# Optimization experiments

Hardware: AMD Instinct MI355X
Metric: run time of the kernel (lower is better)

## Reference

```python
import jax, jax.numpy as jnp
import numpy as np

V, D, L, H, FF, MAXLEN, M = 128, 512, 4, 8, 2048, 1024, 4
B, T = 2, 1024
DK = D // H
EPS = 1e-5  # F.layer_norm default


def setup_inputs() -> dict:
    key = jax.random.key(0)
    ks = jax.random.split(key, 10)
    x = jax.random.randint(ks[0], (B, T), 0, V)
    inp = {
        'x': x,
        'tok_emb': 0.02 * jax.random.normal(ks[1], (M, V, D), jnp.float32),
        'pos_emb': 0.02 * jax.random.normal(ks[2], (M, MAXLEN, D), jnp.float32),
        'ln1_w': jnp.ones((L, M, D), jnp.float32),
        'ln1_b': jnp.zeros((L, M, D), jnp.float32),
        'qkv_w': jax.random.normal(ks[3], (L, M, 3 * D, D), jnp.float32) * (1.0 / np.sqrt(D)),
        'qkv_b': jnp.zeros((L, M, 3 * D), jnp.float32),
        'out_w': jax.random.normal(ks[4], (L, M, D, D), jnp.float32) * (1.0 / np.sqrt(D)),
        'out_b': jnp.zeros((L, M, D), jnp.float32),
        'ln2_w': jnp.ones((L, M, D), jnp.float32),
        'ln2_b': jnp.zeros((L, M, D), jnp.float32),
        'ff1_w': jax.random.normal(ks[5], (L, M, FF, D), jnp.float32) * (1.0 / np.sqrt(D)),
        'ff1_b': jnp.zeros((L, M, FF), jnp.float32),
        'ff2_w': jax.random.normal(ks[6], (L, M, D, FF), jnp.float32) * (1.0 / np.sqrt(FF)),
        'ff2_b': jnp.zeros((L, M, D), jnp.float32),
        'lnf_w': jnp.ones((M, D), jnp.float32),
        'lnf_b': jnp.zeros((M, D), jnp.float32),
        'head_w': jax.random.normal(ks[7], (M, V, D), jnp.float32) * (1.0 / np.sqrt(D)),
        'head_b': jnp.zeros((M, V), jnp.float32),
    }
    return inp


def _layernorm(h, w, b):
    # h: [M,B,T,D], w/b: [M,D]
    mu = h.mean(-1, keepdims=True)
    var = ((h - mu) ** 2).mean(-1, keepdims=True)
    return (h - mu) / jnp.sqrt(var + EPS) * w[:, None, None, :] + b[:, None, None, :]


def reference(x, tok_emb, pos_emb, ln1_w, ln1_b, qkv_w, qkv_b, out_w, out_b,
              ln2_w, ln2_b, ff1_w, ff1_b, ff2_w, ff2_b, lnf_w, lnf_b, head_w, head_b):
    Bx, Tx = x.shape
    # token + positional embedding, batched over the model axis -> [M,B,T,D]
    h = tok_emb[:, x] + pos_emb[:, None, :Tx, :]
    mask = jnp.tril(jnp.ones((Tx, Tx), bool))  # causal
    scale = 1.0 / np.sqrt(DK).astype(np.float32)
    for l in range(L):
        n = _layernorm(h, ln1_w[l], ln1_b[l])
        qkv = jnp.einsum('mbtd,mfd->mbtf', n, qkv_w[l]) + qkv_b[l][:, None, None, :]
        # (M,B,T,H,3*DK) -> (M,B,H,T,3*DK); chunk last dim into q,k,v (matches torch chunk)
        qkv = qkv.reshape(h.shape[0], Bx, Tx, H, 3 * DK).transpose(0, 1, 3, 2, 4)
        q, k, v = jnp.split(qkv, 3, axis=-1)
        s = jnp.einsum('mbhtd,mbhsd->mbhts', q, k) * scale
        s = jnp.where(mask, s, -jnp.inf)
        a = jax.nn.softmax(s, axis=-1)
        o = jnp.einsum('mbhts,mbhsd->mbhtd', a, v)
        o = o.transpose(0, 1, 3, 2, 4).reshape(h.shape[0], Bx, Tx, D)
        o = jnp.einsum('mbtd,med->mbte', o, out_w[l]) + out_b[l][:, None, None, :]
        h = h + o
        n = _layernorm(h, ln2_w[l], ln2_b[l])
        f = jax.nn.relu(jnp.einsum('mbtd,mfd->mbtf', n, ff1_w[l]) + ff1_b[l][:, None, None, :])
        f = jnp.einsum('mbtf,mdf->mbtd', f, ff2_w[l]) + ff2_b[l][:, None, None, :]
        h = h + f
    h = _layernorm(h, lnf_w, lnf_b)
    logits = jnp.einsum('mbtd,mvd->mbtv', h, head_w) + head_b[:, None, None, :]
    return logits.transpose(1, 0, 2, 3)  # (B, model_count, T, V) like torch.stack(dim=1)
```

## Files before the change

### kernel.cpp

```cpp
#include <hip/hip_runtime.h>

#define M_  4
#define B_  2
#define T_  1024
#define D_  512
#define V_  128
#define L_  4
#define H_  8
#define FF_ 2048
#define DK_ 64
#define BT_ (B_*T_)
#define EPS_ 1e-5f
#define QSCALE_ 0.18033688f

typedef __attribute__((ext_vector_type(8))) short  bf16x8;
typedef __attribute__((ext_vector_type(4))) float  f32x4;
typedef __attribute__((ext_vector_type(8))) ushort ushort8v;

__device__ __forceinline__ float b2f(ushort u) {
  union { unsigned int i; float f; } c; c.i = ((unsigned int)u) << 16; return c.f;
}
__device__ __forceinline__ ushort f2b(float f) {
  union { float f; unsigned int i; } c; c.f = f;
  return (ushort)((c.i + 0x7FFFu + ((c.i >> 16) & 1u)) >> 16);
}
__device__ __forceinline__ void gload_lds16(const void* g, void* l) {
  __builtin_amdgcn_global_load_lds((const __attribute__((address_space(1))) unsigned int*)g,
                                   (__attribute__((address_space(3))) unsigned int*)l, 16, 0, 0);
}

__global__ __launch_bounds__(128)
void k_embed(const int* __restrict__ x, const float* __restrict__ tok,
             const float* __restrict__ pos, ushort* __restrict__ h)
{
  const int t = blockIdx.x, b = blockIdx.y, m = blockIdx.z;
  const int d = threadIdx.x * 4;
  const int xv = x[b*T_ + t];
  const float4 tv = *(const float4*)&tok[((size_t)m*V_ + xv)*D_ + d];
  const float4 pv = *(const float4*)&pos[((size_t)m*1024 + t)*D_ + d];
  ushort4 r;
  r.x = f2b(tv.x + pv.x); r.y = f2b(tv.y + pv.y);
  r.z = f2b(tv.z + pv.z); r.w = f2b(tv.w + pv.w);
  *(ushort4*)&h[(((size_t)m*B_ + b)*T_ + t)*D_ + d] = r;
}

#define NQ4_ 786432
#define NO4_ 262144
#define NF4_ 1048576
#define LBLK_ 12288
#define LSLAB_ 12582912
__global__ __launch_bounds__(256)
void k_cvt_all(const float* __restrict__ qkv_w, const float* __restrict__ out_w,
               const float* __restrict__ ff1_w, const float* __restrict__ ff2_w,
               const float* __restrict__ head_w, ushort* __restrict__ wall)
{
  const int bx = blockIdx.x;
  const float* s; ushort* d;
  long i;
  if (bx < 4*LBLK_) {
    const int l  = bx / LBLK_;
    i = (long)(bx % LBLK_)*256 + threadIdx.x;
    ushort* base = wall + (size_t)l*LSLAB_;
    if (i < NQ4_)                  { s = qkv_w + (size_t)l*3145728; d = base; }
    else if (i < NQ4_+NO4_)        { s = out_w + (size_t)l*1048576; d = base + 3145728; i -= NQ4_; }
    else if (i < NQ4_+NO4_+NF4_)   { s = ff1_w + (size_t)l*4194304; d = base + 4194304; i -= NQ4_+NO4_; }
    else                           { s = ff2_w + (size_t)l*4194304; d = base + 8388608; i -= NQ4_+NO4_+NF4_; }
  } else {
    i = (long)(bx - 4*LBLK_)*256 + threadIdx.x;
    s = head_w; d = wall + (size_t)4*LSLAB_;
  }
  const float4 a = ((const float4*)s)[i];
  ushort4 o;
  o.x = f2b(a.x); o.y = f2b(a.y); o.z = f2b(a.z); o.w = f2b(a.w);
  ((ushort4*)d)[i] = o;
}

__global__ __launch_bounds__(256)
void k_ln(const ushort* __restrict__ x, const float* __restrict__ w,
          const float* __restrict__ bb, ushort* __restrict__ y)
{
  const int row  = blockIdx.x * 4 + (threadIdx.x >> 6);
  const int lane = threadIdx.x & 63;
  const int m = row >> 11;
  const ushort8v xv = *(const ushort8v*)&x[(size_t)row*D_ + lane*8];
  float v[8];
  #pragma unroll
  for (int k = 0; k < 8; ++k) v[k] = b2f(xv[k]);
  float s = 0.f, s2 = 0.f;
  #pragma unroll
  for (int k = 0; k < 8; ++k) { s += v[k]; s2 += v[k]*v[k]; }
  #pragma unroll
  for (int off = 1; off < 64; off <<= 1) {
    s  += __shfl_xor(s, off);
    s2 += __shfl_xor(s2, off);
  }
  const float mu   = s * (1.0f/D_);
  const float var  = s2 * (1.0f/D_) - mu*mu;
  const float rstd = rsqrtf(var + EPS_);
  const float* wp = w + m*D_ + lane*8;
  const float* bp = bb + m*D_ + lane*8;
  const float4 w0 = *(const float4*)wp, w1 = *(const float4*)(wp+4);
  const float4 b0 = *(const float4*)bp, b1 = *(const float4*)(bp+4);
  const float wr[8] = {w0.x,w0.y,w0.z,w0.w,w1.x,w1.y,w1.z,w1.w};
  const float br[8] = {b0.x,b0.y,b0.z,b0.w,b1.x,b1.y,b1.z,b1.w};
  ushort8v o;
  #pragma unroll
  for (int k = 0; k < 8; ++k) o[k] = f2b((v[k]-mu)*rstd*wr[k] + br[k]);
  *(ushort8v*)&y[(size_t)row*D_ + lane*8] = o;
}

template<int OUTBF, int ACT, int RES, int HEADOUT, int SPLITV>
__global__ __launch_bounds__(256)
void k_gemm(const ushort* __restrict__ A, const ushort* __restrict__ W,
            const float* __restrict__ bias, const ushort* __restrict__ resid,
            void* __restrict__ C, ushort* __restrict__ vt, int RR, int NN, int KK)
{
  const int m  = blockIdx.z;
  const int r0 = blockIdx.x * 128;
  const int c0 = blockIdx.y * 128;
  const ushort* Am = A + (size_t)m*RR*KK;
  const ushort* Wm = W + (size_t)m*NN*KK;

  __shared__ ushort As[2][128*64];
  __shared__ ushort Bs[2][128*64];

  const int tid  = threadIdx.x;
  const int lane = tid & 63;
  const int wave = tid >> 6;
  const int wr = wave >> 1, wc = wave & 1;
  const int fr = lane & 15;
  const int fq = lane >> 4;

  f32x4 acc[4][4];
  #pragma unroll
  for (int i = 0; i < 4; ++i)
    #pragma unroll
    for (int j = 0; j < 4; ++j)
      acc[i][j] = (f32x4){0.f,0.f,0.f,0.f};

  #pragma unroll
  for (int i = 0; i < 4; ++i) {
    const int c = i*256 + tid;
    const int row = c >> 3, ch = c & 7;
    const int sch = ch ^ (row & 7);
    gload_lds16(Am + (size_t)(r0+row)*KK + sch*8, (ushort*)As[0] + (size_t)c*8);
    gload_lds16(Wm + (size_t)(c0+row)*KK + sch*8, (ushort*)Bs[0] + (size_t)c*8);
  }
  __syncthreads();

  const int NK = KK >> 6;
  for (int kt = 0; kt < NK; ++kt) {
    const int cur = kt & 1;

    if (kt + 1 < NK) {
      const int k0 = (kt + 1) * 64;
      #pragma unroll
      for (int i = 0; i < 4; ++i) {
        const int c = i*256 + tid;
        const int row = c >> 3, ch = c & 7;
        const int sch = ch ^ (row & 7);
        gload_lds16(Am + (size_t)(r0+row)*KK + k0 + sch*8, (ushort*)As[cur^1] + (size_t)c*8);
        gload_lds16(Wm + (size_t)(c0+row)*KK + k0 + sch*8, (ushort*)Bs[cur^1] + (size_t)c*8);
      }
      asm volatile("s_waitcnt vmcnt(8)" ::: "memory");
    } else {
      asm volatile("s_waitcnt vmcnt(0)" ::: "memory");
    }
    __builtin_amdgcn_sched_barrier(0);
    __builtin_amdgcn_s_barrier();

    #pragma unroll
    for (int kk = 0; kk < 2; ++kk) {
      bf16x8 af[4], bfv[4];
      #pragma unroll
      for (int i = 0; i < 4; ++i) {
        const int rowA = wr*64 + i*16 + fr;
        af[i]  = *(const bf16x8*)&As[cur][rowA*64 + (((kk*4 + fq) ^ (rowA & 7))*8)];
        const int rowB = wc*64 + i*16 + fr;
        bfv[i] = *(const bf16x8*)&Bs[cur][rowB*64 + (((kk*4 + fq) ^ (rowB & 7))*8)];
      }
      #pragma unroll
      for (int i = 0; i < 4; ++i)
        #pragma unroll
        for (int j = 0; j < 4; ++j)
          acc[i][j] = __builtin_amdgcn_mfma_f32_16x16x32_bf16(af[i], bfv[j], acc[i][j], 0, 0, 0);
    }
    __builtin_amdgcn_s_barrier();
  }

  const int colb = c0 + wc*64 + fr;
  float bi[4];
  #pragma unroll
  for (int j = 0; j < 4; ++j) bi[j] = bias[(size_t)m*NN + colb + j*16];

  if (SPLITV) {
    #pragma unroll
    for (int i = 0; i < 4; ++i) {
      const int row0 = r0 + wr*64 + i*16 + fq*4;
      const int mbg = (blockIdx.z)*B_ + (row0 >> 10);
      const int t0  = row0 & 1023;
      #pragma unroll
      for (int j = 0; j < 4; ++j) {
        const int col = colb + j*16;
        const int hh2 = col / 192;
        const int sub = col - hh2*192;
        float v0 = acc[i][j][0] + bi[j];
        float v1 = acc[i][j][1] + bi[j];
        float v2 = acc[i][j][2] + bi[j];
        float v3 = acc[i][j][3] + bi[j];
        if (sub >= 128) {
          ushort4 pk;
          pk.x = f2b(v0); pk.y = f2b(v1); pk.z = f2b(v2); pk.w = f2b(v3);
          *(ushort4*)&vt[(((size_t)mbg*8 + hh2)*64 + (sub-128))*1024 + t0] = pk;
        } else {
          if (sub < 64) { v0 *= QSCALE_; v1 *= QSCALE_; v2 *= QSCALE_; v3 *= QSCALE_; }
          ushort* cp = (ushort*)C + ((size_t)m*RR + row0)*NN + col;
          cp[0*NN] = f2b(v0); cp[1*NN] = f2b(v1); cp[2*NN] = f2b(v2); cp[3*NN] = f2b(v3);
        }
      }
    }
  } else {
    #pragma unroll
    for (int i = 0; i < 4; ++i) {
      #pragma unroll
      for (int r = 0; r < 4; ++r) {
        const int row = r0 + wr*64 + i*16 + fq*4 + r;
        #pragma unroll
        for (int j = 0; j < 4; ++j) {
          float val = acc[i][j][r] + bi[j];
          if (ACT) val = fmaxf(val, 0.0f);
          const int col = colb + j*16;
          size_t oidx;
          if (HEADOUT) {
            const int b = row >> 10, t = row & 1023;
            oidx = (((size_t)b*M_ + m)*T_ + t)*V_ + col;
          } else {
            oidx = ((size_t)m*RR + row)*NN + col;
          }
          float v2 = val;
          if (RES) v2 += b2f(resid[oidx]);
          if (OUTBF) ((ushort*)C)[oidx] = f2b(v2);
          else       ((float*)C)[oidx]  = v2;
        }
      }
    }
  }
}

__global__ __launch_bounds__(256)
void k_attn_mfma(const ushort* __restrict__ qkvb, const ushort* __restrict__ vt,
                 ushort* __restrict__ o)
{
  const int hh   = blockIdx.x;
  const int pair = blockIdx.y;
  const int mbg  = blockIdx.z;

  __shared__ ushort Qs[64*64];
  __shared__ ushort Ks[2][64*64];
  __shared__ ushort Vs[2][64*64];
  __shared__ ushort Ps[4][16*80];

  const int tid  = threadIdx.x;
  const int lane = tid & 63;
  const int wave = tid >> 6;
  const int fr = lane & 15;
  const int fq = lane >> 4;

  const ushort* qk_base = qkvb + (size_t)mbg*T_*(3*D_) + hh*(3*DK_);
  const ushort* vt_base = vt + ((size_t)(mbg*8 + hh)*64)*1024;

  #pragma unroll 1
  for (int pass = 0; pass < 2; ++pass) {
    const int qb = pass ? (15 - pair) : pair;

    #pragma unroll
    for (int i = 0; i < 2; ++i) {
      const int c = wave*128 + i*64 + lane;
      const int row = c >> 3, ch = c & 7;
      const int sch = (ch ^ (row & 7)) * 8;
      gload_lds16(qk_base + (size_t)(qb*64 + row)*(3*D_) + sch,
                  (ushort*)Qs + (size_t)(wave*128 + i*64)*8);
      gload_lds16(qk_base + (size_t)row*(3*D_) + DK_ + sch,
                  (ushort*)Ks[0] + (size_t)(wave*128 + i*64)*8);
      gload_lds16(vt_base + (size_t)row*1024 + sch,
                  (ushort*)Vs[0] + (size_t)(wave*128 + i*64)*8);
    }
    __syncthreads();

    bf16x8 aQ[2];
    #pragma unroll
    for (int kc = 0; kc < 2; ++kc) {
      const int qrow = wave*16 + fr;
      aQ[kc] = *(const bf16x8*)&Qs[qrow*64 + (((kc*4 + fq) ^ (qrow&7))*8)];
    }

    float m_q = -3.0e38f, l_q = 0.0f;
    f32x4 Of[4];
    #pragma unroll
    for (int j = 0; j < 4; ++j) Of[j] = (f32x4){0.f,0.f,0.f,0.f};

    const int qrow_abs0 = qb*64 + wave*16 + fq*4;

    auto tile = [&](int kb, bool DIAG, bool PRE) {
      const int cur = kb & 1;
      if (PRE) {
        #pragma unroll
        for (int i = 0; i < 2; ++i) {
          const int c = wave*128 + i*64 + lane;
          const int row = c >> 3, ch = c & 7;
          const int sch = (ch ^ (row & 7)) * 8;
          gload_lds16(qk_base + (size_t)((kb+1)*64 + row)*(3*D_) + DK_ + sch,
                      (ushort*)Ks[cur^1] + (size_t)(wave*128 + i*64)*8);
          gload_lds16(vt_base + (size_t)row*1024 + (kb+1)*64 + sch,
                      (ushort*)Vs[cur^1] + (size_t)(wave*128 + i*64)*8);
        }
        asm volatile("s_waitcnt vmcnt(4)" ::: "memory");
      } else {
        asm volatile("s_waitcnt vmcnt(0)" ::: "memory");
      }
      __builtin_amdgcn_sched_barrier(0);
      __builtin_amdgcn_s_barrier();

      f32x4 acc[4];
      #pragma unroll
      for (int j = 0; j < 4; ++j) acc[j] = (f32x4){0.f,0.f,0.f,0.f};
      __builtin_amdgcn_s_setprio(1);
      #pragma unroll
      for (int kc = 0; kc < 2; ++kc) {
        #pragma unroll
        for (int j = 0; j < 4; ++j) {
          const int krow = j*16 + fr;
          const bf16x8 bK = *(const bf16x8*)&Ks[cur][krow*64 + (((kc*4 + fq) ^ (krow&7))*8)];
          acc[j] = __builtin_amdgcn_mfma_f32_16x16x32_bf16(bK, aQ[kc], acc[j], 0, 0, 0);
        }
      }
      __builtin_amdgcn_s_setprio(0);

      float sv[16];
      #pragma unroll
      for (int j = 0; j < 4; ++j)
        #pragma unroll
        for (int r = 0; r < 4; ++r) {
          float v = acc[j][r];
          if (DIAG && (j*16 + fq*4 + r) > (wave*16 + fr)) v = -3.0e38f;
          sv[j*4+r] = v;
        }
      float a0 = fmaxf(fmaxf(sv[0],  sv[1]),  sv[2]);
      float a1 = fmaxf(fmaxf(sv[3],  sv[4]),  sv[5]);
      float a2 = fmaxf(fmaxf(sv[6],  sv[7]),  sv[8]);
      float a3 = fmaxf(fmaxf(sv[9],  sv[10]), sv[11]);
      float a4 = fmaxf(fmaxf(sv[12], sv[13]), sv[14]);
      float rm = fmaxf(fmaxf(fmaxf(a0, a1), fmaxf(a2, a3)), fmaxf(a4, sv[15]));
      rm = fmaxf(rm, __shfl_xor(rm, 16));
      rm = fmaxf(rm, __shfl_xor(rm, 32));
      if (!__all(rm - m_q <= 8.0f)) {
        const float mn = fmaxf(m_q, rm);
        const float sc = exp2f(m_q - mn);
        m_q = mn;
        l_q *= sc;
        float scr[4];
        #pragma unroll
        for (int r = 0; r < 4; ++r) scr[r] = __shfl(sc, fq*4 + r);
        #pragma unroll
        for (int j = 0; j < 4; ++j)
          #pragma unroll
          for (int r = 0; r < 4; ++r) Of[j][r] *= scr[r];
      }
      float p[16];
      #pragma unroll
      for (int i2 = 0; i2 < 16; ++i2) p[i2] = exp2f(sv[i2] - m_q);
      float s0 = (p[0]+p[1]) + (p[2]+p[3]);
      float s1 = (p[4]+p[5]) + (p[6]+p[7]);
      float s2 = (p[8]+p[9]) + (p[10]+p[11]);
      float s3 = (p[12]+p[13]) + (p[14]+p[15]);
      float rs = (s0+s1) + (s2+s3);
      rs += __shfl_xor(rs, 16);
      rs += __shfl_xor(rs, 32);
      l_q += rs;

      #pragma unroll
      for (int j = 0; j < 4; ++j) {
        unsigned int lo, hi;
        asm("v_cvt_pk_bf16_f32 %0, %1, %2" : "=v"(lo) : "v"(p[j*4+0]), "v"(p[j*4+1]));
        asm("v_cvt_pk_bf16_f32 %0, %1, %2" : "=v"(hi) : "v"(p[j*4+2]), "v"(p[j*4+3]));
        const int idx = (fr*80 + j*16 + fq*4) ^ ((fr>>2)<<4);
        *(unsigned int*)&Ps[wave][idx]     = lo;
        *(unsigned int*)&Ps[wave][idx + 2] = hi;
      }

      __builtin_amdgcn_s_setprio(1);
      #pragma unroll
      for (int kc = 0; kc < 2; ++kc) {
        const int pidx = fr*80 + kc*32 + fq*8;
        const bf16x8 pa = *(const bf16x8*)&Ps[wave][pidx ^ ((fr>>2)<<4)];
        #pragma unroll
        for (int j = 0; j < 4; ++j) {
          const int vrow = j*16 + fr;
          const bf16x8 bV = *(const bf16x8*)&Vs[cur][vrow*64 + (((kc*4 + fq) ^ (vrow&7))*8)];
          Of[j] = __builtin_amdgcn_mfma_f32_16x16x32_bf16(pa, bV, Of[j], 0, 0, 0);
        }
      }
      __builtin_amdgcn_s_setprio(0);
      __builtin_amdgcn_s_barrier();
    };

    for (int kb = 0; kb < qb; ++kb) tile(kb, false, true);
    tile(qb, true, false);

    const float linv = 1.0f / l_q;
    float inv[4];
    #pragma unroll
    for (int r = 0; r < 4; ++r) inv[r] = __shfl(linv, fq*4 + r);
    #pragma unroll
    for (int r = 0; r < 4; ++r) {
      ushort* op = o + ((size_t)mbg*T_ + (qrow_abs0 + r))*D_ + hh*DK_ + fr;
      #pragma unroll
      for (int j = 0; j < 4; ++j)
        op[j*16] = f2b(Of[j][r] * inv[r]);
    }
  }
}

extern "C" void kernel_launch(void* const* d_in, const int* in_sizes, int n_in,
                              void* d_out, int out_size, void* d_ws, size_t ws_size,
                              hipStream_t stream)
{
  const int*   x       = (const int*)  d_in[0];
  const float* tok_emb = (const float*)d_in[1];
  const float* pos_emb = (const float*)d_in[2];
  const float* ln1_w   = (const float*)d_in[3];
  const float* ln1_b   = (const float*)d_in[4];
  const float* qkv_w   = (const float*)d_in[5];
  const float* qkv_b   = (const float*)d_in[6];
  const float* out_w   = (const float*)d_in[7];
  const float* out_b   = (const float*)d_in[8];
  const float* ln2_w   = (const float*)d_in[9];
  const float* ln2_b   = (const float*)d_in[10];
  const float* ff1_w   = (const float*)d_in[11];
  const float* ff1_b   = (const float*)d_in[12];
  const float* ff2_w   = (const float*)d_in[13];
  const float* ff2_b   = (const float*)d_in[14];
  const float* lnf_w   = (const float*)d_in[15];
  const float* lnf_b   = (const float*)d_in[16];
  const float* head_w  = (const float*)d_in[17];
  const float* head_b  = (const float*)d_in[18];
  float* outp = (float*)d_out;

  const size_t HS = (size_t)M_*B_*T_*D_;
  ushort* h     = (ushort*)d_ws;
  ushort* nb    = h + HS;
  ushort* qkvb  = nb + HS;
  ushort* ob    = qkvb + (size_t)M_*B_*T_*3*D_;
  ushort* fb    = qkvb;
  ushort* vtb   = ob + HS;
  ushort* wall  = vtb + HS;
  ushort* wh    = wall + (size_t)4*LSLAB_;

  const int ROWS = M_*B_*T_;

  k_cvt_all<<<4*LBLK_ + 256, 256, 0, stream>>>(qkv_w, out_w, ff1_w, ff2_w, head_w, wall);
  k_embed<<<dim3(T_, B_, M_), 128, 0, stream>>>(x, tok_emb, pos_emb, h);

  for (int l = 0; l < L_; ++l) {
    ushort* wq  = wall + (size_t)l*LSLAB_;
    ushort* wo  = wq  + 3145728;
    ushort* wf1 = wo  + 1048576;
    ushort* wf2 = wf1 + 4194304;

    k_ln<<<ROWS/4, 256, 0, stream>>>(h, ln1_w + l*M_*D_, ln1_b + l*M_*D_, nb);

    k_gemm<1,0,0,0,1><<<dim3(BT_/128, (3*D_)/128, M_), 256, 0, stream>>>(
        nb, wq, qkv_b + l*M_*3*D_, nullptr, qkvb, vtb, BT_, 3*D_, D_);

    k_attn_mfma<<<dim3(H_, T_/128, M_*B_), 256, 0, stream>>>(qkvb, vtb, ob);

    k_gemm<1,0,1,0,0><<<dim3(BT_/128, D_/128, M_), 256, 0, stream>>>(
        ob, wo, out_b + l*M_*D_, h, h, nullptr, BT_, D_, D_);

    k_ln<<<ROWS/4, 256, 0, stream>>>(h, ln2_w + l*M_*D_, ln2_b + l*M_*D_, nb);

    k_gemm<1,1,0,0,0><<<dim3(BT_/128, FF_/128, M_), 256, 0, stream>>>(
        nb, wf1, ff1_b + l*M_*FF_, nullptr, fb, nullptr, BT_, FF_, D_);

    k_gemm<1,0,1,0,0><<<dim3(BT_/128, D_/128, M_), 256, 0, stream>>>(
        fb, wf2, ff2_b + l*M_*D_, h, h, nullptr, BT_, D_, FF_);
  }

  k_ln<<<ROWS/4, 256, 0, stream>>>(h, lnf_w, lnf_b, nb);
  k_gemm<0,0,0,1,0><<<dim3(BT_/128, V_/128, M_), 256, 0, stream>>>(
      nb, wh, head_b, nullptr, outp, nullptr, BT_, V_, D_);
}
```

Measured before the change: 580.1 us.

## Fuse fp32-to-bf16 weight conversion into GEMM B-tile loading

Removes the separate up-front kernel that converted all weights to bf16. Each GEMM now loads fp32 weight tiles into registers, converts them, and writes them to LDS after the MFMA stage, while A tiles still go direct to LDS. This drops one full read and write pass over all weights. In exchange, each GEMM block reads twice the weight bytes, and the register staging adds pressure and waitcnt complexity; weights are re-read once per row block.

Measured after the change: 744.8 us. +28.4%, slower.

```diff
diff --git a/kernel.cpp b/kernel.cpp
--- a/kernel.cpp
+++ b/kernel.cpp
@@ -42,37 +42,6 @@
   r.x = f2b(tv.x + pv.x); r.y = f2b(tv.y + pv.y);
   r.z = f2b(tv.z + pv.z); r.w = f2b(tv.w + pv.w);
   *(ushort4*)&h[(((size_t)m*B_ + b)*T_ + t)*D_ + d] = r;
-}
-
-#define NQ4_ 786432
-#define NO4_ 262144
-#define NF4_ 1048576
-#define LBLK_ 12288
-#define LSLAB_ 12582912
-__global__ __launch_bounds__(256)
-void k_cvt_all(const float* __restrict__ qkv_w, const float* __restrict__ out_w,
-               const float* __restrict__ ff1_w, const float* __restrict__ ff2_w,
-               const float* __restrict__ head_w, ushort* __restrict__ wall)
-{
-  const int bx = blockIdx.x;
-  const float* s; ushort* d;
-  long i;
-  if (bx < 4*LBLK_) {
-    const int l  = bx / LBLK_;
-    i = (long)(bx % LBLK_)*256 + threadIdx.x;
-    ushort* base = wall + (size_t)l*LSLAB_;
-    if (i < NQ4_)                  { s = qkv_w + (size_t)l*3145728; d = base; }
-    else if (i < NQ4_+NO4_)        { s = out_w + (size_t)l*1048576; d = base + 3145728; i -= NQ4_; }
-    else if (i < NQ4_+NO4_+NF4_)   { s = ff1_w + (size_t)l*4194304; d = base + 4194304; i -= NQ4_+NO4_; }
-    else                           { s = ff2_w + (size_t)l*4194304; d = base + 8388608; i -= NQ4_+NO4_+NF4_; }
-  } else {
-    i = (long)(bx - 4*LBLK_)*256 + threadIdx.x;
-    s = head_w; d = wall + (size_t)4*LSLAB_;
-  }
-  const float4 a = ((const float4*)s)[i];
-  ushort4 o;
-  o.x = f2b(a.x); o.y = f2b(a.y); o.z = f2b(a.z); o.w = f2b(a.w);
-  ((ushort4*)d)[i] = o;
 }
 
 __global__ __launch_bounds__(256)
@@ -111,7 +80,7 @@
 
 template<int OUTBF, int ACT, int RES, int HEADOUT, int SPLITV>
 __global__ __launch_bounds__(256)
-void k_gemm(const ushort* __restrict__ A, const ushort* __restrict__ W,
+void k_gemm(const ushort* __restrict__ A, const float* __restrict__ W,
             const float* __restrict__ bias, const ushort* __restrict__ resid,
             void* __restrict__ C, ushort* __restrict__ vt, int RR, int NN, int KK)
 {
@@ -119,7 +88,7 @@
   const int r0 = blockIdx.x * 128;
   const int c0 = blockIdx.y * 128;
   const ushort* Am = A + (size_t)m*RR*KK;
-  const ushort* Wm = W + (size_t)m*NN*KK;
+  const float*  Wm = W + (size_t)m*NN*KK;
 
   __shared__ ushort As[2][128*64];
   __shared__ ushort Bs[2][128*64];
@@ -138,34 +107,62 @@
     for (int j = 0; j < 4; ++j)
       acc[i][j] = (f32x4){0.f,0.f,0.f,0.f};
 
-  #pragma unroll
-  for (int i = 0; i < 4; ++i) {
-    const int c = i*256 + tid;
-    const int row = c >> 3, ch = c & 7;
-    const int sch = ch ^ (row & 7);
-    gload_lds16(Am + (size_t)(r0+row)*KK + sch*8, (ushort*)As[0] + (size_t)c*8);
-    gload_lds16(Wm + (size_t)(c0+row)*KK + sch*8, (ushort*)Bs[0] + (size_t)c*8);
-  }
-  __syncthreads();
+  float4 br[8];
+
+  auto issueA = [&](int kt, int buf) {
+    const int k0 = kt * 64;
+    #pragma unroll
+    for (int i = 0; i < 4; ++i) {
+      const int c = i*256 + tid;
+      const int row = c >> 3, ch = c & 7;
+      const int sch = ch ^ (row & 7);
+      gload_lds16(Am + (size_t)(r0+row)*KK + k0 + sch*8, (ushort*)As[buf] + (size_t)c*8);
+    }
+  };
+  auto issueB = [&](int kt) {
+    const int k0 = kt * 64;
+    #pragma unroll
+    for (int i = 0; i < 4; ++i) {
+      const int c = i*256 + tid;
+      const int row = c >> 3, ch = c & 7;
+      const int sch = ch ^ (row & 7);
+      const float* p = Wm + (size_t)(c0+row)*KK + k0 + sch*8;
+      br[2*i]   = *(const float4*)p;
+      br[2*i+1] = *(const float4*)(p + 4);
+    }
+  };
+  auto writeB = [&](int buf) {
+    #pragma unroll
+    for (int i = 0; i < 4; ++i) {
+      const int c = i*256 + tid;
+      ushort8v t;
+      t[0]=f2b(br[2*i].x);   t[1]=f2b(br[2*i].y);
+      t[2]=f2b(br[2*i].z);   t[3]=f2b(br[2*i].w);
+      t[4]=f2b(br[2*i+1].x); t[5]=f2b(br[2*i+1].y);
+      t[6]=f2b(br[2*i+1].z); t[7]=f2b(br[2*i+1].w);
+      *(ushort8v*)&Bs[buf][(size_t)c*8] = t;
+    }
+  };
+
+  issueB(0);
+  __builtin_amdgcn_sched_barrier(0);
+  issueA(0, 0);
+  asm volatile("s_waitcnt vmcnt(4)" ::: "memory");
+  writeB(0);
 
   const int NK = KK >> 6;
   for (int kt = 0; kt < NK; ++kt) {
     const int cur = kt & 1;
 
     if (kt + 1 < NK) {
-      const int k0 = (kt + 1) * 64;
-      #pragma unroll
-      for (int i = 0; i < 4; ++i) {
-        const int c = i*256 + tid;
-        const int row = c >> 3, ch = c & 7;
-        const int sch = ch ^ (row & 7);
-        gload_lds16(Am + (size_t)(r0+row)*KK + k0 + sch*8, (ushort*)As[cur^1] + (size_t)c*8);
-        gload_lds16(Wm + (size_t)(c0+row)*KK + k0 + sch*8, (ushort*)Bs[cur^1] + (size_t)c*8);
-      }
-      asm volatile("s_waitcnt vmcnt(8)" ::: "memory");
+      issueB(kt + 1);
+      __builtin_amdgcn_sched_barrier(0);
+      issueA(kt + 1, cur ^ 1);
+      asm volatile("s_waitcnt vmcnt(12)" ::: "memory");
     } else {
       asm volatile("s_waitcnt vmcnt(0)" ::: "memory");
     }
+    asm volatile("s_waitcnt lgkmcnt(0)" ::: "memory");
     __builtin_amdgcn_sched_barrier(0);
     __builtin_amdgcn_s_barrier();
 
@@ -186,6 +183,11 @@
           acc[i][j] = __builtin_amdgcn_mfma_f32_16x16x32_bf16(af[i], bfv[j], acc[i][j], 0, 0, 0);
     }
     __builtin_amdgcn_s_barrier();
+
+    if (kt + 1 < NK) {
+      asm volatile("s_waitcnt vmcnt(4)" ::: "memory");
+      writeB(cur ^ 1);
+    }
   }
 
   const int colb = c0 + wc*64 + fr;
@@ -453,40 +455,32 @@
   ushort* ob    = qkvb + (size_t)M_*B_*T_*3*D_;
   ushort* fb    = qkvb;
   ushort* vtb   = ob + HS;
-  ushort* wall  = vtb + HS;
-  ushort* wh    = wall + (size_t)4*LSLAB_;
 
   const int ROWS = M_*B_*T_;
 
-  k_cvt_all<<<4*LBLK_ + 256, 256, 0, stream>>>(qkv_w, out_w, ff1_w, ff2_w, head_w, wall);
   k_embed<<<dim3(T_, B_, M_), 128, 0, stream>>>(x, tok_emb, pos_emb, h);
 
   for (int l = 0; l < L_; ++l) {
-    ushort* wq  = wall + (size_t)l*LSLAB_;
-    ushort* wo  = wq  + 3145728;
-    ushort* wf1 = wo  + 1048576;
-    ushort* wf2 = wf1 + 4194304;
-
     k_ln<<<ROWS/4, 256, 0, stream>>>(h, ln1_w + l*M_*D_, ln1_b + l*M_*D_, nb);
 
     k_gemm<1,0,0,0,1><<<dim3(BT_/128, (3*D_)/128, M_), 256, 0, stream>>>(
-        nb, wq, qkv_b + l*M_*3*D_, nullptr, qkvb, vtb, BT_, 3*D_, D_);
+        nb, qkv_w + (size_t)l*M_*3*D_*D_, qkv_b + l*M_*3*D_, nullptr, qkvb, vtb, BT_, 3*D_, D_);
 
     k_attn_mfma<<<dim3(H_, T_/128, M_*B_), 256, 0, stream>>>(qkvb, vtb, ob);
 
     k_gemm<1,0,1,0,0><<<dim3(BT_/128, D_/128, M_), 256, 0, stream>>>(
-        ob, wo, out_b + l*M_*D_, h, h, nullptr, BT_, D_, D_);
+        ob, out_w + (size_t)l*M_*D_*D_, out_b + l*M_*D_, h, h, nullptr, BT_, D_, D_);
 
     k_ln<<<ROWS/4, 256, 0, stream>>>(h, ln2_w + l*M_*D_, ln2_b + l*M_*D_, nb);
 
     k_gemm<1,1,0,0,0><<<dim3(BT_/128, FF_/128, M_), 256, 0, stream>>>(
-        nb, wf1, ff1_b + l*M_*FF_, nullptr, fb, nullptr, BT_, FF_, D_);
+        nb, ff1_w + (size_t)l*M_*FF_*D_, ff1_b + l*M_*FF_, nullptr, fb, nullptr, BT_, FF_, D_);
 
     k_gemm<1,0,1,0,0><<<dim3(BT_/128, D_/128, M_), 256, 0, stream>>>(
-        fb, wf2, ff2_b + l*M_*D_, h, h, nullptr, BT_, D_, FF_);
+        fb, ff2_w + (size_t)l*M_*D_*FF_, ff2_b + l*M_*D_, h, h, nullptr, BT_, D_, FF_);
   }
 
   k_ln<<<ROWS/4, 256, 0, stream>>>(h, lnf_w, lnf_b, nb);
   k_gemm<0,0,0,1,0><<<dim3(BT_/128, V_/128, M_), 256, 0, stream>>>(
-      nb, wh, head_b, nullptr, outp, nullptr, BT_, V_, D_);
-}
+      nb, head_w, head_b, nullptr, outp, nullptr, BT_, V_, D_);
+}
```
